# Performance work log

Hardware: AMD Instinct MI355X
Metric: run time of the kernel (lower is better)

## Reference

```python
import jax, jax.numpy as jnp
import numpy as np

N_WIRES = 4
BATCH, SEQ, EMBED, FFN = 8, 512, 512, 2048


def setup_inputs() -> dict:
    key = jax.random.key(0)
    k_x, k_w1, k_w2 = jax.random.split(key, 3)
    x = jax.random.normal(k_x, (BATCH, SEQ, EMBED), dtype=jnp.float32)
    # Linear params (torch Linear: y = x @ W^T + b; we store pre-transposed)
    W1 = jax.random.normal(k_w1, (EMBED, FFN), dtype=jnp.float32) / np.sqrt(EMBED)
    b1 = jnp.zeros((FFN,), dtype=jnp.float32)
    W2 = jax.random.normal(k_w2, (FFN, EMBED), dtype=jnp.float32) / np.sqrt(FFN)
    b2 = jnp.zeros((EMBED,), dtype=jnp.float32)
    return {"x": x, "W1": W1, "b1": b1, "W2": W2, "b2": b2}


def reference(x, W1, b1, W2, b2):
    b, s, d = x.shape
    flat = x.reshape(b * s, d)                      # [n, d], n = b*s
    # Quantum kernel: circuit RY(x_i) then RY(-y_i) per wire on |0..0>;
    # |0..0> amplitude = prod_i cos((x_i - y_i)/2); only first n_wires feats used
    # (reset_states(1) + states.view(-1)[0] selects batch row 0 of the reshape).
    f = flat[:, :N_WIRES]                           # [n, nw]
    half_diff = (f[:, None, :] - f[None, :, :]) * 0.5   # [n, n, nw]
    gram = jnp.abs(jnp.prod(jnp.cos(half_diff), axis=-1))  # [n, n]
    out = gram @ flat                               # [n, d]
    h = jax.nn.relu(out @ W1 + b1)                  # [n, ffn]  (dropout = eval identity)
    y = h @ W2 + b2                                 # [n, d]
    return y.reshape(b, s, d)
```

## Files before the change

### kernel.cpp

```cpp
#include <hip/hip_runtime.h>
#include <hip/hip_bf16.h>
#include <stdint.h>

using bf = __bf16;
typedef __attribute__((ext_vector_type(8))) __bf16 bf16x8;
typedef __attribute__((ext_vector_type(4))) float f32x4;
typedef __attribute__((ext_vector_type(4))) int i32x4;

#define M_TOT 4096
#define D_EMB 512
#define F_FFN 2048

__device__ __forceinline__ void gload_lds16(const void* g, void* l) {
  __builtin_amdgcn_global_load_lds(
      (const __attribute__((address_space(1))) uint32_t*)g,
      (__attribute__((address_space(3))) uint32_t*)l, 16, 0, 0);
}

__device__ __forceinline__ int swz128(int row, int b) {
  return row * 128 + (b ^ ((row & 7) << 4));
}
__device__ __forceinline__ bf16x8 ldf128(const char* base, int row, int b) {
  return *(const bf16x8*)(base + swz128(row, b));
}
__device__ __forceinline__ i32x4 ldf128i(const char* base, int row, int b) {
  return *(const i32x4*)(base + swz128(row, b));
}
template <int CHUNKS>
__device__ __forceinline__ void stage_rows8(const void* gsrc, size_t ld_bytes, char* lbase,
                                            int wave, int lane) {
  const int rsub = lane >> 3, csub = lane & 7;
  const int sc = csub ^ rsub;
#pragma unroll
  for (int i = 0; i < CHUNKS / 8; ++i) {
    int chunk = wave + i * 8;
    int row = chunk * 8 + rsub;
    gload_lds16((const char*)gsrc + (size_t)row * ld_bytes + sc * 16, lbase + chunk * 1024);
  }
}
template <int CHUNKS>
__device__ __forceinline__ void stage_rows4(const void* gsrc, size_t ld_bytes, char* lbase,
                                            int wave, int lane) {
  const int rsub = lane >> 3, csub = lane & 7;
  const int sc = csub ^ rsub;
#pragma unroll
  for (int i = 0; i < CHUNKS / 4; ++i) {
    int chunk = wave + i * 4;
    int row = chunk * 8 + rsub;
    gload_lds16((const char*)gsrc + (size_t)row * ld_bytes + sc * 16, lbase + chunk * 1024);
  }
}

__device__ __forceinline__ int quant_i8(float x, float s) {
  float v = x * s;
  v = fminf(127.f, fmaxf(-127.f, v));
  return (int)rintf(v);
}

#define NB_SGEN 1024
#define NT_FT   2048
#define NT_W1   1024
#define NT_W2   1024

__global__ __launch_bounds__(256) void k_prep(const float* __restrict__ x,
                                              const float* __restrict__ W1,
                                              const float* __restrict__ W2,
                                              int8_t* __restrict__ fi8, bf* __restrict__ w1T,
                                              bf* __restrict__ w2T, int8_t* __restrict__ S) {
  __shared__ __align__(16) char smem[32768];
  const int bid = blockIdx.x, tid = threadIdx.x;

  if (bid < NB_SGEN) {
    char* phiL = smem;
    char* st = smem + 16384;
    const int m0 = (bid & 31) * 128;
    const int j0 = (bid >> 5) * 128;
    {
      int g = (tid < 128) ? (m0 + tid) : (j0 + tid - 128);
      float c[4], s[4];
#pragma unroll
      for (int k = 0; k < 4; ++k) {
        float f = x[(size_t)g * D_EMB + k] * 0.5f;
        sincosf(f, &s[k], &c[k]);
      }
      bf* row = (bf*)(phiL + tid * 64);
#pragma unroll
      for (int m = 0; m < 16; ++m) {
        float p = 1.0f;
#pragma unroll
        for (int k = 0; k < 4; ++k) p *= ((m >> k) & 1) ? s[k] : c[k];
        row[m] = (bf)p;
      }
#pragma unroll
      for (int m = 16; m < 32; ++m) row[m] = (bf)0.0f;
    }
    __syncthreads();

    const int wave = tid >> 6, lane = tid & 63;
    const int lr = lane & 15, lg = lane >> 4;
    const bf16x8 a0 = *(const bf16x8*)(phiL + (wave * 32 + lr) * 64 + lg * 16);
    const bf16x8 a1 = *(const bf16x8*)(phiL + (wave * 32 + 16 + lr) * 64 + lg * 16);

    const int mb0 = wave * 32 + lg * 4;
    const int key = (lr & 7) << 4;
#pragma unroll
    for (int jf = 0; jf < 8; ++jf) {
      bf16x8 b = *(const bf16x8*)(phiL + (128 + jf * 16 + lr) * 64 + lg * 16);
      f32x4 s0 = __builtin_amdgcn_mfma_f32_16x16x32_bf16(a0, b, f32x4{0.f, 0.f, 0.f, 0.f}, 0, 0, 0);
      f32x4 s1 = __builtin_amdgcn_mfma_f32_16x16x32_bf16(a1, b, f32x4{0.f, 0.f, 0.f, 0.f}, 0, 0, 0);
      uint32_t w0 = 0, w1 = 0;
#pragma unroll
      for (int r = 0; r < 4; ++r) {
        uint32_t q0 = (uint32_t)min(127, (int)rintf(fabsf(s0[r]) * 127.f));
        uint32_t q1 = (uint32_t)min(127, (int)rintf(fabsf(s1[r]) * 127.f));
        w0 |= q0 << (8 * r);
        w1 |= q1 << (8 * r);
      }
      int jrow = jf * 16 + lr;
      *(uint32_t*)(st + jrow * 128 + (mb0 ^ key)) = w0;
      *(uint32_t*)(st + jrow * 128 + ((mb0 + 16) ^ key)) = w1;
    }
    __syncthreads();
#pragma unroll
    for (int i = 0; i < 4; ++i) {
      int idx = tid + i * 256;
      int jrow = idx >> 3, seg = idx & 7;
      i32x4 v = *(const i32x4*)(st + jrow * 128 + ((seg * 16) ^ ((jrow & 7) << 4)));
      *(i32x4*)(S + (size_t)(j0 + jrow) * M_TOT + m0 + seg * 16) = v;
    }
    return;
  }

  float(*tile)[33] = (float(*)[33])smem;
  const int tx = tid & 31, ty = tid >> 5;
  if (bid < NB_SGEN + NT_FT) {
    int b2 = bid - NB_SGEN;
    int c0 = (b2 % (D_EMB / 32)) * 32, r0 = (b2 / (D_EMB / 32)) * 32;
#pragma unroll
    for (int i = 0; i < 32; i += 8)
      tile[ty + i][tx] = x[(size_t)(r0 + ty + i) * D_EMB + c0 + tx];
    __syncthreads();
#pragma unroll
    for (int i = 0; i < 32; i += 8)
      fi8[(size_t)(c0 + ty + i) * M_TOT + r0 + tx] = (int8_t)quant_i8(tile[tx][ty + i], 15.875f);
  } else if (bid < NB_SGEN + NT_FT + NT_W1) {
    int b2 = bid - NB_SGEN - NT_FT;
    int c0 = (b2 % (F_FFN / 32)) * 32, r0 = (b2 / (F_FFN / 32)) * 32;
#pragma unroll
    for (int i = 0; i < 32; i += 8)
      tile[ty + i][tx] = W1[(size_t)(r0 + ty + i) * F_FFN + c0 + tx];
    __syncthreads();
#pragma unroll
    for (int i = 0; i < 32; i += 8)
      w1T[(size_t)(c0 + ty + i) * D_EMB + r0 + tx] = (bf)tile[tx][ty + i];
  } else {
    int b2 = bid - NB_SGEN - NT_FT - NT_W1;
    int c0 = (b2 % (D_EMB / 32)) * 32, r0 = (b2 / (D_EMB / 32)) * 32;
#pragma unroll
    for (int i = 0; i < 32; i += 8)
      tile[ty + i][tx] = W2[(size_t)(r0 + ty + i) * D_EMB + c0 + tx];
    __syncthreads();
#pragma unroll
    for (int i = 0; i < 32; i += 8)
      w2T[(size_t)(c0 + ty + i) * F_FFN + r0 + tx] = (bf)tile[tx][ty + i];
  }
}

__global__ __launch_bounds__(512, 1) void k_gemmi8(const int8_t* __restrict__ S,
                                                   const int8_t* __restrict__ FT,
                                                   bf* __restrict__ outb) {
  constexpr int ABUF = 64 * 128, BBUF = 128 * 128, BUF = ABUF + BBUF;
  __shared__ __align__(16) char sm[3 * BUF];

  const int tid = threadIdx.x;
  const int wave = tid >> 6, lane = tid & 63;
  const int lr = lane & 15, lg = lane >> 4;
  const int wm = wave & 1, wn = (wave >> 1) & 1, ks = wave >> 2;

  const int lin = blockIdx.x;
  const int e = lin & 7, jj = lin >> 3;
  const int bm = e * 8 + (jj >> 2), bn = jj & 3;
  const int m0 = bm * 64, n0 = bn * 128;

  i32x4 acc[2][4];
#pragma unroll
  for (int i = 0; i < 2; ++i)
#pragma unroll
    for (int f = 0; f < 4; ++f) acc[i][f] = i32x4{0, 0, 0, 0};

  stage_rows8<8>(S + (size_t)m0 * M_TOT, M_TOT, sm, wave, lane);
  stage_rows8<16>(FT + (size_t)n0 * M_TOT, M_TOT, sm + ABUF, wave, lane);
  stage_rows8<8>(S + (size_t)m0 * M_TOT + 128, M_TOT, sm + BUF, wave, lane);
  stage_rows8<16>(FT + (size_t)n0 * M_TOT + 128, M_TOT, sm + BUF + ABUF, wave, lane);

  constexpr int NT = M_TOT / 128;
  for (int t = 0; t < NT; ++t) {
    char* aTc = sm + (t % 3) * BUF;
    char* bTc = aTc + ABUF;
    if (t + 1 < NT) asm volatile("s_waitcnt vmcnt(3)" ::: "memory");
    else            asm volatile("s_waitcnt vmcnt(0)" ::: "memory");
    __builtin_amdgcn_s_barrier();

    if (t + 2 < NT) {
      char* aTn = sm + ((t + 2) % 3) * BUF;
      stage_rows8<8>(S + (size_t)m0 * M_TOT + (t + 2) * 128, M_TOT, aTn, wave, lane);
      stage_rows8<16>(FT + (size_t)n0 * M_TOT + (t + 2) * 128, M_TOT, aTn + ABUF, wave, lane);
    }
    i32x4 a[2], b[4];
#pragma unroll
    for (int i = 0; i < 2; ++i) a[i] = ldf128i(aTc, wm * 32 + i * 16 + lr, ks * 64 + lg * 16);
#pragma unroll
    for (int f = 0; f < 4; ++f) b[f] = ldf128i(bTc, wn * 64 + f * 16 + lr, ks * 64 + lg * 16);
#pragma unroll
    for (int i = 0; i < 2; ++i)
#pragma unroll
      for (int f = 0; f < 4; ++f)
        acc[i][f] = __builtin_amdgcn_mfma_i32_16x16x64_i8(a[i], b[f], acc[i][f], 0, 0, 0);
  }

  __syncthreads();
  if (ks == 1) {
    char* dst = sm + (wave - 4) * 8192 + lane * 128;
#pragma unroll
    for (int i = 0; i < 2; ++i)
#pragma unroll
      for (int f = 0; f < 4; ++f) *(i32x4*)(dst + (i * 4 + f) * 16) = acc[i][f];
  }
  __syncthreads();
  if (ks == 0) {
    const char* src = sm + wave * 8192 + lane * 128;
    constexpr float SCALE = 8.0f / 16129.0f;
#pragma unroll
    for (int i = 0; i < 2; ++i)
#pragma unroll
      for (int f = 0; f < 4; ++f) {
        i32x4 p = *(const i32x4*)(src + (i * 4 + f) * 16);
        int n = n0 + wn * 64 + f * 16 + lr;
#pragma unroll
        for (int r = 0; r < 4; ++r) {
          int m = m0 + wm * 32 + i * 16 + lg * 4 + r;
          outb[(size_t)m * D_EMB + n] = (bf)((float)(acc[i][f][r] + p[r]) * SCALE);
        }
      }
  }
}

__global__ __launch_bounds__(256, 2) void k_gemm4(const bf* __restrict__ A, const bf* __restrict__ BT,
                                                  const float* __restrict__ bias, bf* __restrict__ out,
                                                  int M, int N, int K) {
  constexpr int BM = 128, BN = 64;
  constexpr int ABUF = BM * 128, BBUF = BN * 128, BUF = ABUF + BBUF;
  __shared__ __align__(16) char sm[3 * BUF];

  const int tid = threadIdx.x;
  const int wave = tid >> 6, lane = tid & 63;
  const int lr = lane & 15, lg = lane >> 4;
  const int wm = wave >> 1, wn = wave & 1;

  const int lin = blockIdx.x;
  const int e = lin & 7, jj = lin >> 3;
  const int bm = e * 4 + (jj & 3), bn = jj >> 2;
  const int m0 = bm * BM, n0 = bn * BN;

  f32x4 acc[4][2];
#pragma unroll
  for (int i = 0; i < 4; ++i)
#pragma unroll
    for (int f = 0; f < 2; ++f) acc[i][f] = f32x4{0.f, 0.f, 0.f, 0.f};

  stage_rows4<16>(A + (size_t)m0 * K, (size_t)K * 2, sm, wave, lane);
  stage_rows4<8>(BT + (size_t)n0 * K, (size_t)K * 2, sm + ABUF, wave, lane);
  stage_rows4<16>(A + (size_t)m0 * K + 64, (size_t)K * 2, sm + BUF, wave, lane);
  stage_rows4<8>(BT + (size_t)n0 * K + 64, (size_t)K * 2, sm + BUF + ABUF, wave, lane);

  const int NT = K / 64;
  for (int t = 0; t < NT; ++t) {
    char* aTc = sm + (t % 3) * BUF;
    char* bTc = aTc + ABUF;
    if (t + 1 < NT) asm volatile("s_waitcnt vmcnt(6)" ::: "memory");
    else            asm volatile("s_waitcnt vmcnt(0)" ::: "memory");
    __builtin_amdgcn_s_barrier();

    if (t + 2 < NT) {
      char* aTn = sm + ((t + 2) % 3) * BUF;
      stage_rows4<16>(A + (size_t)m0 * K + (t + 2) * 64, (size_t)K * 2, aTn, wave, lane);
      stage_rows4<8>(BT + (size_t)n0 * K + (t + 2) * 64, (size_t)K * 2, aTn + ABUF, wave, lane);
    }
#pragma unroll
    for (int ksl = 0; ksl < 2; ++ksl) {
      bf16x8 a[4], b[2];
#pragma unroll
      for (int i = 0; i < 4; ++i) a[i] = ldf128(aTc, wm * 64 + i * 16 + lr, (ksl * 32 + lg * 8) * 2);
#pragma unroll
      for (int f = 0; f < 2; ++f) b[f] = ldf128(bTc, wn * 32 + f * 16 + lr, (ksl * 32 + lg * 8) * 2);
#pragma unroll
      for (int i = 0; i < 4; ++i)
#pragma unroll
        for (int f = 0; f < 2; ++f)
          acc[i][f] = __builtin_amdgcn_mfma_f32_16x16x32_bf16(a[i], b[f], acc[i][f], 0, 0, 0);
    }
  }

#pragma unroll
  for (int f = 0; f < 2; ++f) {
    int n = n0 + wn * 32 + f * 16 + lr;
    float bv = bias[n];
#pragma unroll
    for (int i = 0; i < 4; ++i)
#pragma unroll
      for (int r = 0; r < 4; ++r) {
        int m = m0 + wm * 64 + i * 16 + lg * 4 + r;
        float v = acc[i][f][r] + bv;
        v = v > 0.f ? v : 0.f;
        out[(size_t)m * N + n] = (bf)v;
      }
  }
}

template <int BM, int BN, int OUTMODE>
__global__ __launch_bounds__(512, 1) void k_gemm8(const bf* __restrict__ A, const bf* __restrict__ BT,
                                                  const float* __restrict__ bias, void* __restrict__ out,
                                                  int M, int N, int K) {
  constexpr int WN = BN / 2;
  constexpr int FM = 2, FN = WN / 16;
  constexpr int ABUF = BM * 128, BBUF = BN * 128, BUF = ABUF + BBUF;
  constexpr int LP = BM / 64 + BN / 64;
  static_assert(LP == 3 || LP == 4, "vmcnt literal");
  __shared__ __align__(16) char sm[3 * BUF];

  const int tid = threadIdx.x;
  const int wave = tid >> 6, lane = tid & 63;
  const int lr = lane & 15, lg = lane >> 4;
  const int wm = wave >> 1, wn = wave & 1;

  const int lin = blockIdx.x;
  const int e = lin & 7, jj = lin >> 3;
  const int nbn = N / BN;
  const int bm = e * 4 + jj / nbn, bn = jj % nbn;
  const int m0 = bm * BM, n0 = bn * BN;

  f32x4 acc[FM][FN];
#pragma unroll
  for (int i = 0; i < FM; ++i)
#pragma unroll
    for (int f = 0; f < FN; ++f) acc[i][f] = f32x4{0.f, 0.f, 0.f, 0.f};

  stage_rows8<BM / 8>(A + (size_t)m0 * K, (size_t)K * 2, sm, wave, lane);
  stage_rows8<BN / 8>(BT + (size_t)n0 * K, (size_t)K * 2, sm + ABUF, wave, lane);
  stage_rows8<BM / 8>(A + (size_t)m0 * K + 64, (size_t)K * 2, sm + BUF, wave, lane);
  stage_rows8<BN / 8>(BT + (size_t)n0 * K + 64, (size_t)K * 2, sm + BUF + ABUF, wave, lane);

  const int NT = K / 64;
  for (int t = 0; t < NT; ++t) {
    char* aTc = sm + (t % 3) * BUF;
    char* bTc = aTc + ABUF;
    if (t + 1 < NT) {
      if constexpr (LP == 3) asm volatile("s_waitcnt vmcnt(3)" ::: "memory");
      else                   asm volatile("s_waitcnt vmcnt(4)" ::: "memory");
    } else {
      asm volatile("s_waitcnt vmcnt(0)" ::: "memory");
    }
    __builtin_amdgcn_s_barrier();

    if (t + 2 < NT) {
      char* aTn = sm + ((t + 2) % 3) * BUF;
      stage_rows8<BM / 8>(A + (size_t)m0 * K + (t + 2) * 64, (size_t)K * 2, aTn, wave, lane);
      stage_rows8<BN / 8>(BT + (size_t)n0 * K + (t + 2) * 64, (size_t)K * 2, aTn + ABUF, wave, lane);
    }
#pragma unroll
    for (int ksl = 0; ksl < 2; ++ksl) {
      bf16x8 a[FM], b[FN];
#pragma unroll
      for (int i = 0; i < FM; ++i) a[i] = ldf128(aTc, wm * 32 + i * 16 + lr, (ksl * 32 + lg * 8) * 2);
#pragma unroll
      for (int f = 0; f < FN; ++f) b[f] = ldf128(bTc, wn * WN + f * 16 + lr, (ksl * 32 + lg * 8) * 2);
#pragma unroll
      for (int i = 0; i < FM; ++i)
#pragma unroll
        for (int f = 0; f < FN; ++f)
          acc[i][f] = __builtin_amdgcn_mfma_f32_16x16x32_bf16(a[i], b[f], acc[i][f], 0, 0, 0);
    }
  }

#pragma unroll
  for (int f = 0; f < FN; ++f) {
    int n = n0 + wn * WN + f * 16 + lr;
    float bv = (OUTMODE == 2) ? 0.f : bias[n];
#pragma unroll
    for (int i = 0; i < FM; ++i)
#pragma unroll
      for (int r = 0; r < 4; ++r) {
        int m = m0 + wm * 32 + i * 16 + lg * 4 + r;
        float v = acc[i][f][r] + bv;
        if (OUTMODE == 1) {
          v = v > 0.f ? v : 0.f;
          ((bf*)out)[(size_t)m * N + n] = (bf)v;
        } else {
          ((float*)out)[(size_t)m * N + n] = v;
        }
      }
  }
}

constexpr size_t OFF_FI8  = 0;
constexpr size_t OFF_OUTB = OFF_FI8 + (size_t)D_EMB * M_TOT;
constexpr size_t OFF_W1T  = OFF_OUTB + (size_t)M_TOT * D_EMB * 2;
constexpr size_t OFF_W2T  = OFF_W1T + (size_t)F_FFN * D_EMB * 2;
constexpr size_t OFF_S    = OFF_W2T + (size_t)D_EMB * F_FFN * 2;
constexpr size_t OFF_HB   = OFF_S;

extern "C" void kernel_launch(void* const* d_in, const int* in_sizes, int n_in,
                              void* d_out, int out_size, void* d_ws, size_t ws_size,
                              hipStream_t stream) {
  const float* x  = (const float*)d_in[0];
  const float* W1 = (const float*)d_in[1];
  const float* b1 = (const float*)d_in[2];
  const float* W2 = (const float*)d_in[3];
  const float* b2 = (const float*)d_in[4];
  float* y = (float*)d_out;
  char* ws = (char*)d_ws;

  int8_t* fi8 = (int8_t*)(ws + OFF_FI8);
  bf* outb    = (bf*)(ws + OFF_OUTB);
  bf* w1T     = (bf*)(ws + OFF_W1T);
  bf* w2T     = (bf*)(ws + OFF_W2T);
  int8_t* S   = (int8_t*)(ws + OFF_S);
  bf* hb      = (bf*)(ws + OFF_HB);

  k_prep<<<dim3(NB_SGEN + NT_FT + NT_W1 + NT_W2), 256, 0, stream>>>(x, W1, W2, fi8, w1T, w2T, S);

  k_gemmi8<<<dim3(256), 512, 0, stream>>>(S, fi8, outb);

  k_gemm4<<<dim3(1024), 256, 0, stream>>>(outb, w1T, b1, hb, M_TOT, F_FFN, D_EMB);
  k_gemm8<128, 64, 0><<<dim3(256), 512, 0, stream>>>(hb, w2T, b2, (void*)y, M_TOT, D_EMB, F_FFN);
}
```

Baseline: 68.12 us.

## Replace all three GEMMs with uniform 64x64-tile 256-thread kernels

```diff
diff --git a/kernel.cpp b/kernel.cpp
--- a/kernel.cpp
+++ b/kernel.cpp
@@ -25,18 +25,6 @@
 }
 __device__ __forceinline__ i32x4 ldf128i(const char* base, int row, int b) {
   return *(const i32x4*)(base + swz128(row, b));
-}
-template <int CHUNKS>
-__device__ __forceinline__ void stage_rows8(const void* gsrc, size_t ld_bytes, char* lbase,
-                                            int wave, int lane) {
-  const int rsub = lane >> 3, csub = lane & 7;
-  const int sc = csub ^ rsub;
-#pragma unroll
-  for (int i = 0; i < CHUNKS / 8; ++i) {
-    int chunk = wave + i * 8;
-    int row = chunk * 8 + rsub;
-    gload_lds16((const char*)gsrc + (size_t)row * ld_bytes + sc * 16, lbase + chunk * 1024);
-  }
 }
 template <int CHUNKS>
 __device__ __forceinline__ void stage_rows4(const void* gsrc, size_t ld_bytes, char* lbase,
@@ -50,7 +38,6 @@
     gload_lds16((const char*)gsrc + (size_t)row * ld_bytes + sc * 16, lbase + chunk * 1024);
   }
 }
-
 __device__ __forceinline__ int quant_i8(float x, float s) {
   float v = x * s;
   v = fminf(127.f, fmaxf(-127.f, v));
@@ -166,135 +153,57 @@
   }
 }
 
-__global__ __launch_bounds__(512, 1) void k_gemmi8(const int8_t* __restrict__ S,
-                                                   const int8_t* __restrict__ FT,
-                                                   bf* __restrict__ outb) {
-  constexpr int ABUF = 64 * 128, BBUF = 128 * 128, BUF = ABUF + BBUF;
+template <int OUTMODE>
+__global__ __launch_bounds__(256, 3) void k_g64(const bf* __restrict__ A, const bf* __restrict__ BT,
+                                                const float* __restrict__ bias, void* __restrict__ out,
+                                                int N, int K) {
+  constexpr int BUF = 16384;
   __shared__ __align__(16) char sm[3 * BUF];
 
   const int tid = threadIdx.x;
   const int wave = tid >> 6, lane = tid & 63;
   const int lr = lane & 15, lg = lane >> 4;
-  const int wm = wave & 1, wn = (wave >> 1) & 1, ks = wave >> 2;
+  const int wm = wave & 1, wn = wave >> 1;
 
   const int lin = blockIdx.x;
   const int e = lin & 7, jj = lin >> 3;
-  const int bm = e * 8 + (jj >> 2), bn = jj & 3;
-  const int m0 = bm * 64, n0 = bn * 128;
-
-  i32x4 acc[2][4];
+  const int bm = e * 8 + (jj & 7), bn = jj >> 3;
+  const int m0 = bm * 64, n0 = bn * 64;
+
+  f32x4 acc[2][2];
 #pragma unroll
   for (int i = 0; i < 2; ++i)
 #pragma unroll
-    for (int f = 0; f < 4; ++f) acc[i][f] = i32x4{0, 0, 0, 0};
-
-  stage_rows8<8>(S + (size_t)m0 * M_TOT, M_TOT, sm, wave, lane);
-  stage_rows8<16>(FT + (size_t)n0 * M_TOT, M_TOT, sm + ABUF, wave, lane);
-  stage_rows8<8>(S + (size_t)m0 * M_TOT + 128, M_TOT, sm + BUF, wave, lane);
-  stage_rows8<16>(FT + (size_t)n0 * M_TOT + 128, M_TOT, sm + BUF + ABUF, wave, lane);
-
-  constexpr int NT = M_TOT / 128;
-  for (int t = 0; t < NT; ++t) {
-    char* aTc = sm + (t % 3) * BUF;
-    char* bTc = aTc + ABUF;
-    if (t + 1 < NT) asm volatile("s_waitcnt vmcnt(3)" ::: "memory");
-    else            asm volatile("s_waitcnt vmcnt(0)" ::: "memory");
-    __builtin_amdgcn_s_barrier();
-
-    if (t + 2 < NT) {
-      char* aTn = sm + ((t + 2) % 3) * BUF;
-      stage_rows8<8>(S + (size_t)m0 * M_TOT + (t + 2) * 128, M_TOT, aTn, wave, lane);
-      stage_rows8<16>(FT + (size_t)n0 * M_TOT + (t + 2) * 128, M_TOT, aTn + ABUF, wave, lane);
-    }
-    i32x4 a[2], b[4];
-#pragma unroll
-    for (int i = 0; i < 2; ++i) a[i] = ldf128i(aTc, wm * 32 + i * 16 + lr, ks * 64 + lg * 16);
-#pragma unroll
-    for (int f = 0; f < 4; ++f) b[f] = ldf128i(bTc, wn * 64 + f * 16 + lr, ks * 64 + lg * 16);
-#pragma unroll
-    for (int i = 0; i < 2; ++i)
-#pragma unroll
-      for (int f = 0; f < 4; ++f)
-        acc[i][f] = __builtin_amdgcn_mfma_i32_16x16x64_i8(a[i], b[f], acc[i][f], 0, 0, 0);
-  }
-
-  __syncthreads();
-  if (ks == 1) {
-    char* dst = sm + (wave - 4) * 8192 + lane * 128;
-#pragma unroll
-    for (int i = 0; i < 2; ++i)
-#pragma unroll
-      for (int f = 0; f < 4; ++f) *(i32x4*)(dst + (i * 4 + f) * 16) = acc[i][f];
-  }
-  __syncthreads();
-  if (ks == 0) {
-    const char* src = sm + wave * 8192 + lane * 128;
-    constexpr float SCALE = 8.0f / 16129.0f;
-#pragma unroll
-    for (int i = 0; i < 2; ++i)
-#pragma unroll
-      for (int f = 0; f < 4; ++f) {
-        i32x4 p = *(const i32x4*)(src + (i * 4 + f) * 16);
-        int n = n0 + wn * 64 + f * 16 + lr;
-#pragma unroll
-        for (int r = 0; r < 4; ++r) {
-          int m = m0 + wm * 32 + i * 16 + lg * 4 + r;
-          outb[(size_t)m * D_EMB + n] = (bf)((float)(acc[i][f][r] + p[r]) * SCALE);
-        }
-      }
-  }
-}
-
-__global__ __launch_bounds__(256, 2) void k_gemm4(const bf* __restrict__ A, const bf* __restrict__ BT,
-                                                  const float* __restrict__ bias, bf* __restrict__ out,
-                                                  int M, int N, int K) {
-  constexpr int BM = 128, BN = 64;
-  constexpr int ABUF = BM * 128, BBUF = BN * 128, BUF = ABUF + BBUF;
-  __shared__ __align__(16) char sm[3 * BUF];
-
-  const int tid = threadIdx.x;
-  const int wave = tid >> 6, lane = tid & 63;
-  const int lr = lane & 15, lg = lane >> 4;
-  const int wm = wave >> 1, wn = wave & 1;
-
-  const int lin = blockIdx.x;
-  const int e = lin & 7, jj = lin >> 3;
-  const int bm = e * 4 + (jj & 3), bn = jj >> 2;
-  const int m0 = bm * BM, n0 = bn * BN;
-
-  f32x4 acc[4][2];
-#pragma unroll
-  for (int i = 0; i < 4; ++i)
-#pragma unroll
     for (int f = 0; f < 2; ++f) acc[i][f] = f32x4{0.f, 0.f, 0.f, 0.f};
 
-  stage_rows4<16>(A + (size_t)m0 * K, (size_t)K * 2, sm, wave, lane);
-  stage_rows4<8>(BT + (size_t)n0 * K, (size_t)K * 2, sm + ABUF, wave, lane);
-  stage_rows4<16>(A + (size_t)m0 * K + 64, (size_t)K * 2, sm + BUF, wave, lane);
-  stage_rows4<8>(BT + (size_t)n0 * K + 64, (size_t)K * 2, sm + BUF + ABUF, wave, lane);
+  const size_t ldb = (size_t)K * 2;
+  stage_rows4<8>(A + (size_t)m0 * K, ldb, sm, wave, lane);
+  stage_rows4<8>(BT + (size_t)n0 * K, ldb, sm + 8192, wave, lane);
+  stage_rows4<8>(A + (size_t)m0 * K + 64, ldb, sm + BUF, wave, lane);
+  stage_rows4<8>(BT + (size_t)n0 * K + 64, ldb, sm + BUF + 8192, wave, lane);
 
   const int NT = K / 64;
   for (int t = 0; t < NT; ++t) {
     char* aTc = sm + (t % 3) * BUF;
-    char* bTc = aTc + ABUF;
-    if (t + 1 < NT) asm volatile("s_waitcnt vmcnt(6)" ::: "memory");
+    char* bTc = aTc + 8192;
+    if (t + 1 < NT) asm volatile("s_waitcnt vmcnt(4)" ::: "memory");
     else            asm volatile("s_waitcnt vmcnt(0)" ::: "memory");
     __builtin_amdgcn_s_barrier();
 
     if (t + 2 < NT) {
       char* aTn = sm + ((t + 2) % 3) * BUF;
-      stage_rows4<16>(A + (size_t)m0 * K + (t + 2) * 64, (size_t)K * 2, aTn, wave, lane);
-      stage_rows4<8>(BT + (size_t)n0 * K + (t + 2) * 64, (size_t)K * 2, aTn + ABUF, wave, lane);
+      stage_rows4<8>(A + (size_t)m0 * K + (t + 2) * 64, ldb, aTn, wave, lane);
+      stage_rows4<8>(BT + (size_t)n0 * K + (t + 2) * 64, ldb, aTn + 8192, wave, lane);
     }
 #pragma unroll
     for (int ksl = 0; ksl < 2; ++ksl) {
-      bf16x8 a[4], b[2];
-#pragma unroll
-      for (int i = 0; i < 4; ++i) a[i] = ldf128(aTc, wm * 64 + i * 16 + lr, (ksl * 32 + lg * 8) * 2);
+      bf16x8 a[2], b[2];
+#pragma unroll
+      for (int i = 0; i < 2; ++i) a[i] = ldf128(aTc, wm * 32 + i * 16 + lr, (ksl * 32 + lg * 8) * 2);
 #pragma unroll
       for (int f = 0; f < 2; ++f) b[f] = ldf128(bTc, wn * 32 + f * 16 + lr, (ksl * 32 + lg * 8) * 2);
 #pragma unroll
-      for (int i = 0; i < 4; ++i)
+      for (int i = 0; i < 2; ++i)
 #pragma unroll
         for (int f = 0; f < 2; ++f)
           acc[i][f] = __builtin_amdgcn_mfma_f32_16x16x32_bf16(a[i], b[f], acc[i][f], 0, 0, 0);
@@ -306,88 +215,7 @@
     int n = n0 + wn * 32 + f * 16 + lr;
     float bv = bias[n];
 #pragma unroll
-    for (int i = 0; i < 4; ++i)
-#pragma unroll
-      for (int r = 0; r < 4; ++r) {
-        int m = m0 + wm * 64 + i * 16 + lg * 4 + r;
-        float v = acc[i][f][r] + bv;
-        v = v > 0.f ? v : 0.f;
-        out[(size_t)m * N + n] = (bf)v;
-      }
-  }
-}
-
-template <int BM, int BN, int OUTMODE>
-__global__ __launch_bounds__(512, 1) void k_gemm8(const bf* __restrict__ A, const bf* __restrict__ BT,
-                                                  const float* __restrict__ bias, void* __restrict__ out,
-                                                  int M, int N, int K) {
-  constexpr int WN = BN / 2;
-  constexpr int FM = 2, FN = WN / 16;
-  constexpr int ABUF = BM * 128, BBUF = BN * 128, BUF = ABUF + BBUF;
-  constexpr int LP = BM / 64 + BN / 64;
-  static_assert(LP == 3 || LP == 4, "vmcnt literal");
-  __shared__ __align__(16) char sm[3 * BUF];
-
-  const int tid = threadIdx.x;
-  const int wave = tid >> 6, lane = tid & 63;
-  const int lr = lane & 15, lg = lane >> 4;
-  const int wm = wave >> 1, wn = wave & 1;
-
-  const int lin = blockIdx.x;
-  const int e = lin & 7, jj = lin >> 3;
-  const int nbn = N / BN;
-  const int bm = e * 4 + jj / nbn, bn = jj % nbn;
-  const int m0 = bm * BM, n0 = bn * BN;
-
-  f32x4 acc[FM][FN];
-#pragma unroll
-  for (int i = 0; i < FM; ++i)
-#pragma unroll
-    for (int f = 0; f < FN; ++f) acc[i][f] = f32x4{0.f, 0.f, 0.f, 0.f};
-
-  stage_rows8<BM / 8>(A + (size_t)m0 * K, (size_t)K * 2, sm, wave, lane);
-  stage_rows8<BN / 8>(BT + (size_t)n0 * K, (size_t)K * 2, sm + ABUF, wave, lane);
-  stage_rows8<BM / 8>(A + (size_t)m0 * K + 64, (size_t)K * 2, sm + BUF, wave, lane);
-  stage_rows8<BN / 8>(BT + (size_t)n0 * K + 64, (size_t)K * 2, sm + BUF + ABUF, wave, lane);
-
-  const int NT = K / 64;
-  for (int t = 0; t < NT; ++t) {
-    char* aTc = sm + (t % 3) * BUF;
-    char* bTc = aTc + ABUF;
-    if (t + 1 < NT) {
-      if constexpr (LP == 3) asm volatile("s_waitcnt vmcnt(3)" ::: "memory");
-      else                   asm volatile("s_waitcnt vmcnt(4)" ::: "memory");
-    } else {
-      asm volatile("s_waitcnt vmcnt(0)" ::: "memory");
-    }
-    __builtin_amdgcn_s_barrier();
-
-    if (t + 2 < NT) {
-      char* aTn = sm + ((t + 2) % 3) * BUF;
-      stage_rows8<BM / 8>(A + (size_t)m0 * K + (t + 2) * 64, (size_t)K * 2, aTn, wave, lane);
-      stage_rows8<BN / 8>(BT + (size_t)n0 * K + (t + 2) * 64, (size_t)K * 2, aTn + ABUF, wave, lane);
-    }
-#pragma unroll
-    for (int ksl = 0; ksl < 2; ++ksl) {
-      bf16x8 a[FM], b[FN];
-#pragma unroll
-      for (int i = 0; i < FM; ++i) a[i] = ldf128(aTc, wm * 32 + i * 16 + lr, (ksl * 32 + lg * 8) * 2);
-#pragma unroll
-      for (int f = 0; f < FN; ++f) b[f] = ldf128(bTc, wn * WN + f * 16 + lr, (ksl * 32 + lg * 8) * 2);
-#pragma unroll
-      for (int i = 0; i < FM; ++i)
-#pragma unroll
-        for (int f = 0; f < FN; ++f)
-          acc[i][f] = __builtin_amdgcn_mfma_f32_16x16x32_bf16(a[i], b[f], acc[i][f], 0, 0, 0);
-    }
-  }
-
-#pragma unroll
-  for (int f = 0; f < FN; ++f) {
-    int n = n0 + wn * WN + f * 16 + lr;
-    float bv = (OUTMODE == 2) ? 0.f : bias[n];
-#pragma unroll
-    for (int i = 0; i < FM; ++i)
+    for (int i = 0; i < 2; ++i)
 #pragma unroll
       for (int r = 0; r < 4; ++r) {
         int m = m0 + wm * 32 + i * 16 + lg * 4 + r;
@@ -398,6 +226,75 @@
         } else {
           ((float*)out)[(size_t)m * N + n] = v;
         }
+      }
+  }
+}
+
+__global__ __launch_bounds__(256, 3) void k_gi64(const int8_t* __restrict__ S,
+                                                 const int8_t* __restrict__ FT,
+                                                 bf* __restrict__ outb) {
+  constexpr int BUF = 16384;
+  __shared__ __align__(16) char sm[3 * BUF];
+
+  const int tid = threadIdx.x;
+  const int wave = tid >> 6, lane = tid & 63;
+  const int lr = lane & 15, lg = lane >> 4;
+  const int wm = wave & 1, wn = wave >> 1;
+
+  const int lin = blockIdx.x;
+  const int e = lin & 7, jj = lin >> 3;
+  const int bm = e * 8 + (jj & 7), bn = jj >> 3;
+  const int m0 = bm * 64, n0 = bn * 64;
+
+  i32x4 acc[2][2];
+#pragma unroll
+  for (int i = 0; i < 2; ++i)
+#pragma unroll
+    for (int f = 0; f < 2; ++f) acc[i][f] = i32x4{0, 0, 0, 0};
+
+  stage_rows4<8>(S + (size_t)m0 * M_TOT, M_TOT, sm, wave, lane);
+  stage_rows4<8>(FT + (size_t)n0 * M_TOT, M_TOT, sm + 8192, wave, lane);
+  stage_rows4<8>(S + (size_t)m0 * M_TOT + 128, M_TOT, sm + BUF, wave, lane);
+  stage_rows4<8>(FT + (size_t)n0 * M_TOT + 128, M_TOT, sm + BUF + 8192, wave, lane);
+
+  constexpr int NT = M_TOT / 128;
+  for (int t = 0; t < NT; ++t) {
+    char* aTc = sm + (t % 3) * BUF;
+    char* bTc = aTc + 8192;
+    if (t + 1 < NT) asm volatile("s_waitcnt vmcnt(4)" ::: "memory");
+    else            asm volatile("s_waitcnt vmcnt(0)" ::: "memory");
+    __builtin_amdgcn_s_barrier();
+
+    if (t + 2 < NT) {
+      char* aTn = sm + ((t + 2) % 3) * BUF;
+      stage_rows4<8>(S + (size_t)m0 * M_TOT + (t + 2) * 128, M_TOT, aTn, wave, lane);
+      stage_rows4<8>(FT + (size_t)n0 * M_TOT + (t + 2) * 128, M_TOT, aTn + 8192, wave, lane);
+    }
+#pragma unroll
+    for (int ksub = 0; ksub < 2; ++ksub) {
+      i32x4 a[2], b[2];
+#pragma unroll
+      for (int i = 0; i < 2; ++i) a[i] = ldf128i(aTc, wm * 32 + i * 16 + lr, ksub * 64 + lg * 16);
+#pragma unroll
+      for (int f = 0; f < 2; ++f) b[f] = ldf128i(bTc, wn * 32 + f * 16 + lr, ksub * 64 + lg * 16);
+#pragma unroll
+      for (int i = 0; i < 2; ++i)
+#pragma unroll
+        for (int f = 0; f < 2; ++f)
+          acc[i][f] = __builtin_amdgcn_mfma_i32_16x16x64_i8(a[i], b[f], acc[i][f], 0, 0, 0);
+    }
+  }
+
+  constexpr float SCALE = 8.0f / 16129.0f;
+#pragma unroll
+  for (int f = 0; f < 2; ++f) {
+    int n = n0 + wn * 32 + f * 16 + lr;
+#pragma unroll
+    for (int i = 0; i < 2; ++i)
+#pragma unroll
+      for (int r = 0; r < 4; ++r) {
+        int m = m0 + wm * 32 + i * 16 + lg * 4 + r;
+        outb[(size_t)m * D_EMB + n] = (bf)((float)acc[i][f][r] * SCALE);
       }
   }
 }
@@ -429,8 +326,8 @@
 
   k_prep<<<dim3(NB_SGEN + NT_FT + NT_W1 + NT_W2), 256, 0, stream>>>(x, W1, W2, fi8, w1T, w2T, S);
 
-  k_gemmi8<<<dim3(256), 512, 0, stream>>>(S, fi8, outb);
-
-  k_gemm4<<<dim3(1024), 256, 0, stream>>>(outb, w1T, b1, hb, M_TOT, F_FFN, D_EMB);
-  k_gemm8<128, 64, 0><<<dim3(256), 512, 0, stream>>>(hb, w2T, b2, (void*)y, M_TOT, D_EMB, F_FFN);
-}
+  k_gi64<<<dim3(512), 256, 0, stream>>>(S, fi8, outb);
+
+  k_g64<1><<<dim3(2048), 256, 0, stream>>>(outb, w1T, b1, (void*)hb, F_FFN, D_EMB);
+  k_g64<0><<<dim3(512), 256, 0, stream>>>(hb, w2T, b2, (void*)y, D_EMB, F_FFN);
+}
```

Result: no change. 68.36 us (+0.3%).
